# Optimization experiments

Hardware: AMD Instinct MI355X
Metric: run time of the kernel (lower is better)

The kernel has to match this reference:

```python
import jax, jax.numpy as jnp
import numpy as np

NUM_ACTIVE = 2  # num_active from init


def setup_inputs() -> dict:
    key = jax.random.key(0)
    k1, k2, k3, k4 = jax.random.split(key, 4)
    B, S, D, H, E = 2, 1024, 1024, 4096, 8
    x = jax.random.normal(k1, (B, S, D), jnp.float32)
    # router initialized to zeros in the torch module, but we use small random
    # weights so routing is non-degenerate for the correctness baseline
    router_w = jax.random.normal(k2, (D, E), jnp.float32) * 0.02
    router_b = jnp.zeros((E,), jnp.float32)
    w12 = jax.random.normal(k3, (E, D, 2 * H), jnp.float32) * (1.0 / np.sqrt(D))
    w3 = jax.random.normal(k4, (E, H, D), jnp.float32) * (1.0 / np.sqrt(H))
    return {"x": x, "router_w": router_w, "router_b": router_b, "w12": w12, "w3": w3}


def reference(x, router_w, router_b, w12, w3):
    E = router_w.shape[-1]
    # router (eval mode: no jitter noise)
    logits = x @ router_w + router_b                      # [B,S,E]
    scores = jax.nn.sigmoid(logits)
    top_s, top_i = jax.lax.top_k(scores, NUM_ACTIVE)      # [B,S,k]
    rw = top_s / (jnp.sum(top_s, axis=-1, keepdims=True) + 1e-6)
    # per-token combine weight for each expert: sum of routed slot weights
    cw = jnp.sum(jax.nn.one_hot(top_i, E, dtype=x.dtype) * rw[..., None], axis=-2)  # [B,S,E]
    # dense all-expert SwiGLU (same math as masked loop in the original)
    x12 = jnp.einsum('bsd,edh->ebsh', x, w12)             # [E,B,S,2H]
    x1, x2 = jnp.split(x12, 2, axis=-1)
    h = jax.nn.silu(x1) * x2                              # [E,B,S,H]
    out = jnp.einsum('ebsh,ehd,bse->bsd', h, w3, cw)      # [B,S,D]
    aux_loss = 0.01 * jnp.mean(logits ** 2)
    return out, aux_loss
```

## Files before the change

### kernel.cpp

```cpp
#include <hip/hip_runtime.h>
#include <hip/hip_bf16.h>

#define TOK 2048
#define DIM 1024
#define HID 4096
#define NE  8

typedef short bf16x8 __attribute__((ext_vector_type(8)));
typedef float f32x4 __attribute__((ext_vector_type(4)));
typedef unsigned short ushort_t;
typedef unsigned int uint_t;

#define SWZB(n) (((((n) >> 2) ^ ((n) >> 4)) & 3) << 4)

__device__ __forceinline__ ushort_t f2bf(float f) {
  uint_t b = __float_as_uint(f);
  uint_t r = (b + 0x7FFFu + ((b >> 16) & 1u)) >> 16;
  return (ushort_t)r;
}
__device__ __forceinline__ float bf2f(ushort_t u) {
  return __uint_as_float(((uint_t)u) << 16);
}
__device__ __forceinline__ uint_t pk2bf(float a, float b) {
  uint_t r;
  asm("v_cvt_pk_bf16_f32 %0, %1, %2" : "=v"(r) : "v"(a), "v"(b));
  return r;
}

__global__ void router_kernel(const float* __restrict__ x,
                              const float* __restrict__ rw,
                              const float* __restrict__ rb,
                              int* __restrict__ counts,
                              float* __restrict__ tok_ss,
                              int* __restrict__ top_e,
                              float* __restrict__ top_w) {
  const int t = blockIdx.x;
  const int lane = threadIdx.x;
  float acc[NE];
#pragma unroll
  for (int e = 0; e < NE; ++e) acc[e] = 0.f;
  const float* xr = x + (size_t)t * DIM;
  for (int d = lane; d < DIM; d += 64) {
    float xv = xr[d];
    const float* w = rw + (size_t)d * NE;
#pragma unroll
    for (int e = 0; e < NE; ++e) acc[e] += xv * w[e];
  }
#pragma unroll
  for (int e = 0; e < NE; ++e) {
    float v = acc[e];
#pragma unroll
    for (int off = 32; off > 0; off >>= 1) v += __shfl_down(v, off, 64);
    acc[e] = v;
  }
  if (lane == 0) {
    float sc[NE];
    float ss = 0.f;
#pragma unroll
    for (int e = 0; e < NE; ++e) {
      float lg = acc[e] + rb[e];
      ss += lg * lg;
      sc[e] = 1.f / (1.f + expf(-lg));
    }
    tok_ss[t] = ss;
    int i0 = 0;
#pragma unroll
    for (int e = 1; e < NE; ++e) if (sc[e] > sc[i0]) i0 = e;
    int i1 = (i0 == 0) ? 1 : 0;
#pragma unroll
    for (int e = 0; e < NE; ++e) if (e != i0 && sc[e] > sc[i1]) i1 = e;
    float s0 = sc[i0], s1 = sc[i1];
    float inv = 1.f / (s0 + s1 + 1e-6f);
    top_e[t * 2 + 0] = i0;
    top_e[t * 2 + 1] = i1;
    top_w[t * 2 + 0] = s0 * inv;
    top_w[t * 2 + 1] = s1 * inv;
    atomicAdd(&counts[i0], 1);
    atomicAdd(&counts[i1], 1);
  }
}

__global__ void zero_kernel(int* __restrict__ counts) {
  if (threadIdx.x < NE) counts[threadIdx.x] = 0;
}

__global__ void scan_assign_kernel(const int* __restrict__ counts,
                                   const int* __restrict__ top_e,
                                   const float* __restrict__ top_w,
                                   int* __restrict__ offsets,
                                   int* __restrict__ list_tok,
                                   float* __restrict__ list_w,
                                   int* __restrict__ pair_pos) {
  __shared__ int loff[NE + 1];
  __shared__ int lfill[NE];
  if (threadIdx.x == 0) {
    int o = 0;
    for (int e = 0; e < NE; ++e) { loff[e] = o; lfill[e] = o; o += counts[e]; }
    loff[NE] = o;
  }
  __syncthreads();
  if (threadIdx.x <= NE) offsets[threadIdx.x] = loff[threadIdx.x];
  for (int i = threadIdx.x; i < TOK * 2; i += 256) {
    int e = top_e[i];
    int idx = atomicAdd(&lfill[e], 1);
    list_tok[idx] = i >> 1;
    list_w[idx] = top_w[i];
    pair_pos[i] = idx;
  }
}

__global__ void aux_kernel(const float* __restrict__ tok_ss, float* __restrict__ out_aux) {
  __shared__ float sm[256];
  float s = 0.f;
  for (int t = threadIdx.x; t < TOK; t += 256) s += tok_ss[t];
  sm[threadIdx.x] = s;
  __syncthreads();
  for (int w = 128; w > 0; w >>= 1) {
    if (threadIdx.x < w) sm[threadIdx.x] += sm[threadIdx.x + w];
    __syncthreads();
  }
  if (threadIdx.x == 0) *out_aux = 0.01f * sm[0] / (float)(TOK * NE);
}

__global__ void convx_kernel(const float* __restrict__ x, ushort_t* __restrict__ xb) {
  int i = blockIdx.x * 256 + threadIdx.x;
  float4 v = ((const float4*)x)[i];
  uint2 u;
  u.x = pk2bf(v.x, v.y);
  u.y = pk2bf(v.z, v.w);
  ((uint2*)xb)[i] = u;
}

__global__ __launch_bounds__(256)
void gemm1_mfma(const ushort_t* __restrict__ xb,
                const float* __restrict__ w12,
                const int* __restrict__ offsets, const int* __restrict__ list_tok,
                ushort_t* __restrict__ hhi) {
  __shared__ __align__(16) ushort_t Ah[128 * 40];
  __shared__ __align__(16) ushort_t B1[64 * 40];
  __shared__ __align__(16) ushort_t B2[64 * 40];
  __shared__ int stok[128];

  const int e = blockIdx.y >> 4;
  const int rt = blockIdx.y & 15;
  const int rowstart = offsets[e] + rt * 128;
  const int rowend = offsets[e + 1];
  if (rowstart >= rowend) return;
  const int h0 = blockIdx.x * 64;
  const int tid = threadIdx.x;
  const int lane = tid & 63, wid = tid >> 6;
  const int wm = wid >> 1, wn = wid & 1;
  const int lr = lane & 15, kh = lane >> 4;

  if (tid < 128) {
    int r = rowstart + tid;
    stok[tid] = list_tok[r < rowend ? r : rowstart];
  }
  __syncthreads();

  f32x4 acc1[4][2], acc2[4][2];
#pragma unroll
  for (int mi = 0; mi < 4; ++mi)
#pragma unroll
    for (int nj = 0; nj < 2; ++nj) {
      acc1[mi][nj] = (f32x4){0.f, 0.f, 0.f, 0.f};
      acc2[mi][nj] = (f32x4){0.f, 0.f, 0.f, 0.f};
    }

  const int arow0 = tid >> 2, aseg = tid & 3;
  const int arow1 = arow0 + 64;
  const size_t asrc0 = (size_t)stok[arow0] * DIM + aseg * 8;
  const size_t asrc1 = (size_t)stok[arow1] * DIM + aseg * 8;
  const int adst0 = arow0 * 40 + aseg * 8;
  const int adst1 = arow1 * 40 + aseg * 8;

  const int p = tid >> 4, n4 = tid & 15;
  const float* w12e = w12 + (size_t)e * DIM * (2 * HID) + h0 + n4 * 4;
  char* B1c = (char*)B1;
  char* B2c = (char*)B2;

  int boff[2];
#pragma unroll
  for (int nj = 0; nj < 2; ++nj) {
    int n = wn * 32 + nj * 16 + lr;
    boff[nj] = n * 80 + ((kh * 16) ^ SWZB(n));
  }
  int bwoff[4];
#pragma unroll
  for (int c = 0; c < 4; ++c) {
    int n = n4 * 4 + c;
    bwoff[c] = n * 80 + ((4 * p) ^ SWZB(n));
  }

  uint4 ra0, ra1;
  float4 w1a, w1b, w2a, w2b;
#define G1_LOAD(K0) do { \
    ra0 = *(const uint4*)&xb[asrc0 + (K0)]; \
    ra1 = *(const uint4*)&xb[asrc1 + (K0)]; \
    const float* r0 = w12e + (size_t)((K0) + 2 * p) * (2 * HID); \
    w1a = *(const float4*)r0; \
    w1b = *(const float4*)(r0 + 2 * HID); \
    w2a = *(const float4*)(r0 + HID); \
    w2b = *(const float4*)(r0 + HID + 2 * HID); \
  } while (0)

  G1_LOAD(0);
#pragma unroll 1
  for (int k0 = 0; k0 < DIM; k0 += 32) {
    *(uint4*)&Ah[adst0] = ra0;
    *(uint4*)&Ah[adst1] = ra1;
    {
      const float* p1a = (const float*)&w1a;
      const float* p1b = (const float*)&w1b;
      const float* p2a = (const float*)&w2a;
      const float* p2b = (const float*)&w2b;
#pragma unroll
      for (int c = 0; c < 4; ++c) {
        *(uint_t*)(B1c + bwoff[c]) = pk2bf(p1a[c], p1b[c]);
        *(uint_t*)(B2c + bwoff[c]) = pk2bf(p2a[c], p2b[c]);
      }
    }
    __syncthreads();
    if (k0 + 32 < DIM) G1_LOAD(k0 + 32);

    bf16x8 af[4], b1f[2], b2f[2];
#pragma unroll
    for (int mi = 0; mi < 4; ++mi)
      af[mi] = *(bf16x8*)&Ah[(wm * 64 + mi * 16 + lr) * 40 + kh * 8];
#pragma unroll
    for (int nj = 0; nj < 2; ++nj) {
      b1f[nj] = *(bf16x8*)(B1c + boff[nj]);
      b2f[nj] = *(bf16x8*)(B2c + boff[nj]);
    }
#pragma unroll
    for (int mi = 0; mi < 4; ++mi)
#pragma unroll
      for (int nj = 0; nj < 2; ++nj) {
        acc1[mi][nj] = __builtin_amdgcn_mfma_f32_16x16x32_bf16(af[mi], b1f[nj], acc1[mi][nj], 0, 0, 0);
        acc2[mi][nj] = __builtin_amdgcn_mfma_f32_16x16x32_bf16(af[mi], b2f[nj], acc2[mi][nj], 0, 0, 0);
      }
    __syncthreads();
  }
#undef G1_LOAD

#pragma unroll
  for (int mi = 0; mi < 4; ++mi)
#pragma unroll
    for (int nj = 0; nj < 2; ++nj)
#pragma unroll
      for (int r = 0; r < 4; ++r) {
        int row_t = wm * 64 + mi * 16 + kh * 4 + r;
        int gr = rowstart + row_t;
        if (gr < rowend) {
          int col = h0 + wn * 32 + nj * 16 + lr;
          float v1 = acc1[mi][nj][r], v2 = acc2[mi][nj][r];
          float hv = (v1 / (1.f + expf(-v1))) * v2;
          hhi[(size_t)gr * HID + col] = f2bf(hv);
        }
      }
}

__global__ __launch_bounds__(256)
void gemm2_mfma(const ushort_t* __restrict__ hhi,
                const float* __restrict__ w3,
                const int* __restrict__ offsets, const float* __restrict__ list_w,
                ushort_t* __restrict__ pairout) {
  __shared__ __align__(16) ushort_t As0[64 * 40];
  __shared__ __align__(16) ushort_t As1[64 * 40];
  __shared__ __align__(16) ushort_t Bs0[64 * 40];
  __shared__ __align__(16) ushort_t Bs1[64 * 40];

  const int e = blockIdx.y >> 4;
  const int rt = blockIdx.y & 15;
  const int rowstart = offsets[e] + rt * 64;
  const int rowend = offsets[e + 1];
  if (rowstart >= rowend) return;
  const int d0 = blockIdx.x * 64;
  const int tid = threadIdx.x;
  const int lane = tid & 63, wid = tid >> 6;
  const int wm = wid >> 1, wn = wid & 1;
  const int lr = lane & 15, kh = lane >> 4;

  f32x4 acc[2][2];
#pragma unroll
  for (int mi = 0; mi < 2; ++mi)
#pragma unroll
    for (int nj = 0; nj < 2; ++nj) acc[mi][nj] = (f32x4){0.f, 0.f, 0.f, 0.f};

  const int arow = tid >> 2, aseg = tid & 3;
  int gr = rowstart + arow; if (gr >= rowend) gr = rowstart;
  const size_t asrc = (size_t)gr * HID + aseg * 8;
  const int adst = arow * 40 + aseg * 8;

  const int p = tid >> 4, n4 = tid & 15;
  const float* w3e = w3 + (size_t)e * HID * DIM + d0 + n4 * 4;
  char* Bs0c = (char*)Bs0;
  char* Bs1c = (char*)Bs1;

  int boff[2];
#pragma unroll
  for (int nj = 0; nj < 2; ++nj) {
    int n = wn * 32 + nj * 16 + lr;
    boff[nj] = n * 80 + ((kh * 16) ^ SWZB(n));
  }
  int bwoff[4];
#pragma unroll
  for (int c = 0; c < 4; ++c) {
    int n = n4 * 4 + c;
    bwoff[c] = n * 80 + ((4 * p) ^ SWZB(n));
  }

  uint4 ra0, ra1;
  float4 rb00, rb01, rb10, rb11;
#define G2_LOAD(K0) do { \
    ra0 = *(const uint4*)&hhi[asrc + (K0)]; \
    ra1 = *(const uint4*)&hhi[asrc + (K0) + 32]; \
    const float* r0 = w3e + (size_t)((K0) + 2 * p) * DIM; \
    rb00 = *(const float4*)r0; \
    rb01 = *(const float4*)(r0 + DIM); \
    const float* r1 = w3e + (size_t)((K0) + 32 + 2 * p) * DIM; \
    rb10 = *(const float4*)r1; \
    rb11 = *(const float4*)(r1 + DIM); \
  } while (0)

  G2_LOAD(0);
#pragma unroll 1
  for (int k0 = 0; k0 < HID; k0 += 64) {
    *(uint4*)&As0[adst] = ra0;
    *(uint4*)&As1[adst] = ra1;
    {
      const float* pv0 = (const float*)&rb00;
      const float* pv1 = (const float*)&rb01;
      const float* pw0 = (const float*)&rb10;
      const float* pw1 = (const float*)&rb11;
#pragma unroll
      for (int c = 0; c < 4; ++c) {
        *(uint_t*)(Bs0c + bwoff[c]) = pk2bf(pv0[c], pv1[c]);
        *(uint_t*)(Bs1c + bwoff[c]) = pk2bf(pw0[c], pw1[c]);
      }
    }
    __syncthreads();
    if (k0 + 64 < HID) G2_LOAD(k0 + 64);

    {
      bf16x8 af[2], bf[2];
#pragma unroll
      for (int mi = 0; mi < 2; ++mi)
        af[mi] = *(bf16x8*)&As0[(wm * 32 + mi * 16 + lr) * 40 + kh * 8];
#pragma unroll
      for (int nj = 0; nj < 2; ++nj)
        bf[nj] = *(bf16x8*)(Bs0c + boff[nj]);
#pragma unroll
      for (int mi = 0; mi < 2; ++mi)
#pragma unroll
        for (int nj = 0; nj < 2; ++nj)
          acc[mi][nj] = __builtin_amdgcn_mfma_f32_16x16x32_bf16(af[mi], bf[nj], acc[mi][nj], 0, 0, 0);
    }
    {
      bf16x8 af[2], bf[2];
#pragma unroll
      for (int mi = 0; mi < 2; ++mi)
        af[mi] = *(bf16x8*)&As1[(wm * 32 + mi * 16 + lr) * 40 + kh * 8];
#pragma unroll
      for (int nj = 0; nj < 2; ++nj)
        bf[nj] = *(bf16x8*)(Bs1c + boff[nj]);
#pragma unroll
      for (int mi = 0; mi < 2; ++mi)
#pragma unroll
        for (int nj = 0; nj < 2; ++nj)
          acc[mi][nj] = __builtin_amdgcn_mfma_f32_16x16x32_bf16(af[mi], bf[nj], acc[mi][nj], 0, 0, 0);
    }
    __syncthreads();
  }
#undef G2_LOAD

#pragma unroll
  for (int mi = 0; mi < 2; ++mi)
#pragma unroll
    for (int nj = 0; nj < 2; ++nj)
#pragma unroll
      for (int r = 0; r < 4; ++r) {
        int grr = rowstart + wm * 32 + mi * 16 + kh * 4 + r;
        if (grr < rowend) {
          int col = d0 + wn * 32 + nj * 16 + lr;
          pairout[(size_t)grr * DIM + col] = f2bf(acc[mi][nj][r] * list_w[grr]);
        }
      }
}

__global__ void combine_bf(const ushort_t* __restrict__ pairout,
                           const int* __restrict__ pair_pos,
                           float* __restrict__ out) {
  int i = blockIdx.x * 256 + threadIdx.x;
  int t = i >> 8;
  int dv = i & 255;
  int p0 = pair_pos[2 * t], p1 = pair_pos[2 * t + 1];
  ushort4 a = *(const ushort4*)&pairout[(size_t)p0 * DIM + dv * 4];
  ushort4 b = *(const ushort4*)&pairout[(size_t)p1 * DIM + dv * 4];
  float4 o;
  o.x = bf2f(a.x) + bf2f(b.x);
  o.y = bf2f(a.y) + bf2f(b.y);
  o.z = bf2f(a.z) + bf2f(b.z);
  o.w = bf2f(a.w) + bf2f(b.w);
  ((float4*)out)[i] = o;
}

extern "C" void kernel_launch(void* const* d_in, const int* in_sizes, int n_in,
                              void* d_out, int out_size, void* d_ws, size_t ws_size,
                              hipStream_t stream) {
  const float* x   = (const float*)d_in[0];
  const float* rw  = (const float*)d_in[1];
  const float* rb  = (const float*)d_in[2];
  const float* w12 = (const float*)d_in[3];
  const float* w3  = (const float*)d_in[4];
  float* out = (float*)d_out;

  char* ws = (char*)d_ws;
  size_t off = 0;
  auto alloc = [&](size_t bytes) {
    void* p = ws + off;
    off = (off + bytes + 255) & ~255ULL;
    return p;
  };
  int*   counts   = (int*)alloc(NE * 4);
  int*   offsets  = (int*)alloc((NE + 1) * 4);
  float* tok_ss   = (float*)alloc(TOK * 4);
  int*   top_e    = (int*)alloc(TOK * 2 * 4);
  float* top_w    = (float*)alloc(TOK * 2 * 4);
  int*   list_tok = (int*)alloc(TOK * 2 * 4);
  float* list_w   = (float*)alloc(TOK * 2 * 4);
  int*   pair_pos = (int*)alloc(TOK * 2 * 4);

  ushort_t* xb      = (ushort_t*)alloc((size_t)TOK * DIM * 2);
  ushort_t* hhi     = (ushort_t*)alloc((size_t)TOK * 2 * HID * 2);
  ushort_t* pairoutb= (ushort_t*)alloc((size_t)TOK * 2 * DIM * 2);

  hipLaunchKernelGGL(zero_kernel, dim3(1), dim3(64), 0, stream, counts);
  hipLaunchKernelGGL(router_kernel, dim3(TOK), dim3(64), 0, stream,
                     x, rw, rb, counts, tok_ss, top_e, top_w);
  hipLaunchKernelGGL(scan_assign_kernel, dim3(1), dim3(256), 0, stream,
                     counts, top_e, top_w, offsets, list_tok, list_w, pair_pos);
  hipLaunchKernelGGL(aux_kernel, dim3(1), dim3(256), 0, stream,
                     tok_ss, out + (size_t)TOK * DIM);

  hipLaunchKernelGGL(convx_kernel, dim3(TOK * DIM / 4 / 256), dim3(256), 0, stream,
                     x, xb);
  hipLaunchKernelGGL(gemm1_mfma, dim3(HID / 64, NE * 16), dim3(256), 0, stream,
                     xb, w12, offsets, list_tok, hhi);
  hipLaunchKernelGGL(gemm2_mfma, dim3(DIM / 64, NE * 16), dim3(256), 0, stream,
                     hhi, w3, offsets, list_w, pairoutb);
  hipLaunchKernelGGL(combine_bf, dim3(TOK * DIM / 4 / 256), dim3(256), 0, stream,
                     pairoutb, pair_pos, out);
}
```

Before: 341.0 us.

## Double-buffer LDS tiles in both expert GEMM kernels

Both grouped GEMM kernels now keep two LDS buffers for the A and B tiles. Each step computes from the current buffer, then stores the already-prefetched registers into the other buffer and issues the next global load. The goal is to separate LDS writes from MFMA reads and keep loads in flight over more of the loop. The loop still has two barriers per iteration, and the doubled LDS footprint may reduce how many blocks fit on a CU.

```diff
diff --git a/kernel.cpp b/kernel.cpp
--- a/kernel.cpp
+++ b/kernel.cpp
@@ -136,9 +136,9 @@
                 const float* __restrict__ w12,
                 const int* __restrict__ offsets, const int* __restrict__ list_tok,
                 ushort_t* __restrict__ hhi) {
-  __shared__ __align__(16) ushort_t Ah[128 * 40];
-  __shared__ __align__(16) ushort_t B1[64 * 40];
-  __shared__ __align__(16) ushort_t B2[64 * 40];
+  __shared__ __align__(16) ushort_t Ah[2][128 * 40];
+  __shared__ __align__(16) ushort_t B1[2][64 * 40];
+  __shared__ __align__(16) ushort_t B2[2][64 * 40];
   __shared__ int stok[128];
 
   const int e = blockIdx.y >> 4;
@@ -176,8 +176,6 @@
 
   const int p = tid >> 4, n4 = tid & 15;
   const float* w12e = w12 + (size_t)e * DIM * (2 * HID) + h0 + n4 * 4;
-  char* B1c = (char*)B1;
-  char* B2c = (char*)B2;
 
   int boff[2];
 #pragma unroll
@@ -203,34 +201,41 @@
     w2a = *(const float4*)(r0 + HID); \
     w2b = *(const float4*)(r0 + HID + 2 * HID); \
   } while (0)
-
+#define G1_STORE(BUF) do { \
+    *(uint4*)&Ah[BUF][adst0] = ra0; \
+    *(uint4*)&Ah[BUF][adst1] = ra1; \
+    char* b1c = (char*)B1[BUF]; \
+    char* b2c = (char*)B2[BUF]; \
+    const float* p1a = (const float*)&w1a; \
+    const float* p1b = (const float*)&w1b; \
+    const float* p2a = (const float*)&w2a; \
+    const float* p2b = (const float*)&w2b; \
+    _Pragma("unroll") \
+    for (int c = 0; c < 4; ++c) { \
+      *(uint_t*)(b1c + bwoff[c]) = pk2bf(p1a[c], p1b[c]); \
+      *(uint_t*)(b2c + bwoff[c]) = pk2bf(p2a[c], p2b[c]); \
+    } } while (0)
+
+  const int NK = DIM / 32;
   G1_LOAD(0);
+  G1_STORE(0);
+  G1_LOAD(32);
+  __syncthreads();
+  int cur = 0;
+
 #pragma unroll 1
-  for (int k0 = 0; k0 < DIM; k0 += 32) {
-    *(uint4*)&Ah[adst0] = ra0;
-    *(uint4*)&Ah[adst1] = ra1;
-    {
-      const float* p1a = (const float*)&w1a;
-      const float* p1b = (const float*)&w1b;
-      const float* p2a = (const float*)&w2a;
-      const float* p2b = (const float*)&w2b;
-#pragma unroll
-      for (int c = 0; c < 4; ++c) {
-        *(uint_t*)(B1c + bwoff[c]) = pk2bf(p1a[c], p1b[c]);
-        *(uint_t*)(B2c + bwoff[c]) = pk2bf(p2a[c], p2b[c]);
-      }
-    }
-    __syncthreads();
-    if (k0 + 32 < DIM) G1_LOAD(k0 + 32);
-
+  for (int step = 0; step < NK; ++step) {
+    const char* b1r = (const char*)B1[cur];
+    const char* b2r = (const char*)B2[cur];
+    const ushort_t* ahr = Ah[cur];
     bf16x8 af[4], b1f[2], b2f[2];
 #pragma unroll
     for (int mi = 0; mi < 4; ++mi)
-      af[mi] = *(bf16x8*)&Ah[(wm * 64 + mi * 16 + lr) * 40 + kh * 8];
+      af[mi] = *(const bf16x8*)&ahr[(wm * 64 + mi * 16 + lr) * 40 + kh * 8];
 #pragma unroll
     for (int nj = 0; nj < 2; ++nj) {
-      b1f[nj] = *(bf16x8*)(B1c + boff[nj]);
-      b2f[nj] = *(bf16x8*)(B2c + boff[nj]);
+      b1f[nj] = *(const bf16x8*)(b1r + boff[nj]);
+      b2f[nj] = *(const bf16x8*)(b2r + boff[nj]);
     }
 #pragma unroll
     for (int mi = 0; mi < 4; ++mi)
@@ -239,9 +244,16 @@
         acc1[mi][nj] = __builtin_amdgcn_mfma_f32_16x16x32_bf16(af[mi], b1f[nj], acc1[mi][nj], 0, 0, 0);
         acc2[mi][nj] = __builtin_amdgcn_mfma_f32_16x16x32_bf16(af[mi], b2f[nj], acc2[mi][nj], 0, 0, 0);
       }
-    __syncthreads();
+    if (step + 1 < NK) {
+      __syncthreads();
+      G1_STORE(cur ^ 1);
+      if (step + 2 < NK) G1_LOAD((step + 2) * 32);
+      __syncthreads();
+      cur ^= 1;
+    }
   }
 #undef G1_LOAD
+#undef G1_STORE
 
 #pragma unroll
   for (int mi = 0; mi < 4; ++mi)
@@ -265,10 +277,10 @@
                 const float* __restrict__ w3,
                 const int* __restrict__ offsets, const float* __restrict__ list_w,
                 ushort_t* __restrict__ pairout) {
-  __shared__ __align__(16) ushort_t As0[64 * 40];
-  __shared__ __align__(16) ushort_t As1[64 * 40];
-  __shared__ __align__(16) ushort_t Bs0[64 * 40];
-  __shared__ __align__(16) ushort_t Bs1[64 * 40];
+  __shared__ __align__(16) ushort_t As0[2][64 * 40];
+  __shared__ __align__(16) ushort_t As1[2][64 * 40];
+  __shared__ __align__(16) ushort_t Bs0[2][64 * 40];
+  __shared__ __align__(16) ushort_t Bs1[2][64 * 40];
 
   const int e = blockIdx.y >> 4;
   const int rt = blockIdx.y & 15;
@@ -294,8 +306,6 @@
 
   const int p = tid >> 4, n4 = tid & 15;
   const float* w3e = w3 + (size_t)e * HID * DIM + d0 + n4 * 4;
-  char* Bs0c = (char*)Bs0;
-  char* Bs1c = (char*)Bs1;
 
   int boff[2];
 #pragma unroll
@@ -322,34 +332,40 @@
     rb10 = *(const float4*)r1; \
     rb11 = *(const float4*)(r1 + DIM); \
   } while (0)
-
+#define G2_STORE(BUF) do { \
+    *(uint4*)&As0[BUF][adst] = ra0; \
+    *(uint4*)&As1[BUF][adst] = ra1; \
+    char* bs0c = (char*)Bs0[BUF]; \
+    char* bs1c = (char*)Bs1[BUF]; \
+    const float* pv0 = (const float*)&rb00; \
+    const float* pv1 = (const float*)&rb01; \
+    const float* pw0 = (const float*)&rb10; \
+    const float* pw1 = (const float*)&rb11; \
+    _Pragma("unroll") \
+    for (int c = 0; c < 4; ++c) { \
+      *(uint_t*)(bs0c + bwoff[c]) = pk2bf(pv0[c], pv1[c]); \
+      *(uint_t*)(bs1c + bwoff[c]) = pk2bf(pw0[c], pw1[c]); \
+    } } while (0)
+
+  const int NT = HID / 64;
   G2_LOAD(0);
+  G2_STORE(0);
+  G2_LOAD(64);
+  __syncthreads();
+  int cur = 0;
+
 #pragma unroll 1
-  for (int k0 = 0; k0 < HID; k0 += 64) {
-    *(uint4*)&As0[adst] = ra0;
-    *(uint4*)&As1[adst] = ra1;
+  for (int step = 0; step < NT; ++step) {
     {
-      const float* pv0 = (const float*)&rb00;
-      const float* pv1 = (const float*)&rb01;
-      const float* pw0 = (const float*)&rb10;
-      const float* pw1 = (const float*)&rb11;
-#pragma unroll
-      for (int c = 0; c < 4; ++c) {
-        *(uint_t*)(Bs0c + bwoff[c]) = pk2bf(pv0[c], pv1[c]);
-        *(uint_t*)(Bs1c + bwoff[c]) = pk2bf(pw0[c], pw1[c]);
-      }
-    }
-    __syncthreads();
-    if (k0 + 64 < HID) G2_LOAD(k0 + 64);
-
-    {
+      const ushort_t* asr = As0[cur];
+      const char* bsr = (const char*)Bs0[cur];
       bf16x8 af[2], bf[2];
 #pragma unroll
       for (int mi = 0; mi < 2; ++mi)
-        af[mi] = *(bf16x8*)&As0[(wm * 32 + mi * 16 + lr) * 40 + kh * 8];
+        af[mi] = *(const bf16x8*)&asr[(wm * 32 + mi * 16 + lr) * 40 + kh * 8];
 #pragma unroll
       for (int nj = 0; nj < 2; ++nj)
-        bf[nj] = *(bf16x8*)(Bs0c + boff[nj]);
+        bf[nj] = *(const bf16x8*)(bsr + boff[nj]);
 #pragma unroll
       for (int mi = 0; mi < 2; ++mi)
 #pragma unroll
@@ -357,22 +373,31 @@
           acc[mi][nj] = __builtin_amdgcn_mfma_f32_16x16x32_bf16(af[mi], bf[nj], acc[mi][nj], 0, 0, 0);
     }
     {
+      const ushort_t* asr = As1[cur];
+      const char* bsr = (const char*)Bs1[cur];
       bf16x8 af[2], bf[2];
 #pragma unroll
       for (int mi = 0; mi < 2; ++mi)
-        af[mi] = *(bf16x8*)&As1[(wm * 32 + mi * 16 + lr) * 40 + kh * 8];
+        af[mi] = *(const bf16x8*)&asr[(wm * 32 + mi * 16 + lr) * 40 + kh * 8];
 #pragma unroll
       for (int nj = 0; nj < 2; ++nj)
-        bf[nj] = *(bf16x8*)(Bs1c + boff[nj]);
+        bf[nj] = *(const bf16x8*)(bsr + boff[nj]);
 #pragma unroll
       for (int mi = 0; mi < 2; ++mi)
 #pragma unroll
         for (int nj = 0; nj < 2; ++nj)
           acc[mi][nj] = __builtin_amdgcn_mfma_f32_16x16x32_bf16(af[mi], bf[nj], acc[mi][nj], 0, 0, 0);
     }
-    __syncthreads();
+    if (step + 1 < NT) {
+      __syncthreads();
+      G2_STORE(cur ^ 1);
+      if (step + 2 < NT) G2_LOAD((step + 2) * 64);
+      __syncthreads();
+      cur ^= 1;
+    }
   }
 #undef G2_LOAD
+#undef G2_STORE
 
 #pragma unroll
   for (int mi = 0; mi < 2; ++mi)
```

New measurement: 342.0 us. About the same (+0.3%).

## Widen gemm1 N-tile to 128, fuse bf16 conversion into router, drop count kernels

Applied to the files above, without the earlier changes.

gemm1 now computes a 128-wide hidden tile per block instead of 64, doubling the per-block accumulators and B staging in shared memory. Each gathered x tile is reused across twice as many columns, which halves the redundant A reads but raises register pressure. The router kernel now also writes the bf16 copy of x, removing the separate convx launch. Per-expert counts are now computed in shared memory inside scan_assign, removing zero_kernel and the global atomics.

```diff
diff --git a/kernel.cpp b/kernel.cpp
--- a/kernel.cpp
+++ b/kernel.cpp
@@ -30,21 +30,31 @@
 __global__ void router_kernel(const float* __restrict__ x,
                               const float* __restrict__ rw,
                               const float* __restrict__ rb,
-                              int* __restrict__ counts,
                               float* __restrict__ tok_ss,
                               int* __restrict__ top_e,
-                              float* __restrict__ top_w) {
+                              float* __restrict__ top_w,
+                              ushort_t* __restrict__ xb) {
   const int t = blockIdx.x;
   const int lane = threadIdx.x;
   float acc[NE];
 #pragma unroll
   for (int e = 0; e < NE; ++e) acc[e] = 0.f;
-  const float* xr = x + (size_t)t * DIM;
-  for (int d = lane; d < DIM; d += 64) {
-    float xv = xr[d];
-    const float* w = rw + (size_t)d * NE;
-#pragma unroll
-    for (int e = 0; e < NE; ++e) acc[e] += xv * w[e];
+  const float4* x4 = (const float4*)(x + (size_t)t * DIM);
+  uint2* xb2 = (uint2*)(xb + (size_t)t * DIM);
+#pragma unroll
+  for (int j = 0; j < 4; ++j) {
+    int i = j * 64 + lane;
+    float4 v = x4[i];
+    uint2 u;
+    u.x = pk2bf(v.x, v.y);
+    u.y = pk2bf(v.z, v.w);
+    xb2[i] = u;
+    const float* w = rw + (size_t)i * 4 * NE;
+    const float* vp = (const float*)&v;
+#pragma unroll
+    for (int c = 0; c < 4; ++c)
+#pragma unroll
+      for (int e = 0; e < NE; ++e) acc[e] += vp[c] * w[c * NE + e];
   }
 #pragma unroll
   for (int e = 0; e < NE; ++e) {
@@ -75,27 +85,26 @@
     top_e[t * 2 + 1] = i1;
     top_w[t * 2 + 0] = s0 * inv;
     top_w[t * 2 + 1] = s1 * inv;
-    atomicAdd(&counts[i0], 1);
-    atomicAdd(&counts[i1], 1);
-  }
-}
-
-__global__ void zero_kernel(int* __restrict__ counts) {
-  if (threadIdx.x < NE) counts[threadIdx.x] = 0;
-}
-
-__global__ void scan_assign_kernel(const int* __restrict__ counts,
-                                   const int* __restrict__ top_e,
+  }
+}
+
+__global__ void scan_assign_kernel(const int* __restrict__ top_e,
                                    const float* __restrict__ top_w,
                                    int* __restrict__ offsets,
                                    int* __restrict__ list_tok,
                                    float* __restrict__ list_w,
                                    int* __restrict__ pair_pos) {
+  __shared__ int lcount[NE];
   __shared__ int loff[NE + 1];
   __shared__ int lfill[NE];
+  if (threadIdx.x < NE) lcount[threadIdx.x] = 0;
+  __syncthreads();
+  for (int i = threadIdx.x; i < TOK * 2; i += 256)
+    atomicAdd(&lcount[top_e[i]], 1);
+  __syncthreads();
   if (threadIdx.x == 0) {
     int o = 0;
-    for (int e = 0; e < NE; ++e) { loff[e] = o; lfill[e] = o; o += counts[e]; }
+    for (int e = 0; e < NE; ++e) { loff[e] = o; lfill[e] = o; o += lcount[e]; }
     loff[NE] = o;
   }
   __syncthreads();
@@ -122,23 +131,14 @@
   if (threadIdx.x == 0) *out_aux = 0.01f * sm[0] / (float)(TOK * NE);
 }
 
-__global__ void convx_kernel(const float* __restrict__ x, ushort_t* __restrict__ xb) {
-  int i = blockIdx.x * 256 + threadIdx.x;
-  float4 v = ((const float4*)x)[i];
-  uint2 u;
-  u.x = pk2bf(v.x, v.y);
-  u.y = pk2bf(v.z, v.w);
-  ((uint2*)xb)[i] = u;
-}
-
 __global__ __launch_bounds__(256)
 void gemm1_mfma(const ushort_t* __restrict__ xb,
                 const float* __restrict__ w12,
                 const int* __restrict__ offsets, const int* __restrict__ list_tok,
                 ushort_t* __restrict__ hhi) {
   __shared__ __align__(16) ushort_t Ah[128 * 40];
-  __shared__ __align__(16) ushort_t B1[64 * 40];
-  __shared__ __align__(16) ushort_t B2[64 * 40];
+  __shared__ __align__(16) ushort_t B1[128 * 40];
+  __shared__ __align__(16) ushort_t B2[128 * 40];
   __shared__ int stok[128];
 
   const int e = blockIdx.y >> 4;
@@ -146,7 +146,7 @@
   const int rowstart = offsets[e] + rt * 128;
   const int rowend = offsets[e + 1];
   if (rowstart >= rowend) return;
-  const int h0 = blockIdx.x * 64;
+  const int h0 = blockIdx.x * 128;
   const int tid = threadIdx.x;
   const int lane = tid & 63, wid = tid >> 6;
   const int wm = wid >> 1, wn = wid & 1;
@@ -158,11 +158,11 @@
   }
   __syncthreads();
 
-  f32x4 acc1[4][2], acc2[4][2];
+  f32x4 acc1[4][4], acc2[4][4];
 #pragma unroll
   for (int mi = 0; mi < 4; ++mi)
 #pragma unroll
-    for (int nj = 0; nj < 2; ++nj) {
+    for (int nj = 0; nj < 4; ++nj) {
       acc1[mi][nj] = (f32x4){0.f, 0.f, 0.f, 0.f};
       acc2[mi][nj] = (f32x4){0.f, 0.f, 0.f, 0.f};
     }
@@ -179,29 +179,35 @@
   char* B1c = (char*)B1;
   char* B2c = (char*)B2;
 
-  int boff[2];
-#pragma unroll
-  for (int nj = 0; nj < 2; ++nj) {
-    int n = wn * 32 + nj * 16 + lr;
+  int boff[4];
+#pragma unroll
+  for (int nj = 0; nj < 4; ++nj) {
+    int n = wn * 64 + nj * 16 + lr;
     boff[nj] = n * 80 + ((kh * 16) ^ SWZB(n));
   }
-  int bwoff[4];
+  int bwoff[4], bwoff2[4];
 #pragma unroll
   for (int c = 0; c < 4; ++c) {
     int n = n4 * 4 + c;
     bwoff[c] = n * 80 + ((4 * p) ^ SWZB(n));
+    int n2 = 64 + n;
+    bwoff2[c] = n2 * 80 + ((4 * p) ^ SWZB(n2));
   }
 
   uint4 ra0, ra1;
-  float4 w1a, w1b, w2a, w2b;
+  float4 w1a, w1b, w1c, w1d, w2a, w2b, w2c, w2d;
 #define G1_LOAD(K0) do { \
     ra0 = *(const uint4*)&xb[asrc0 + (K0)]; \
     ra1 = *(const uint4*)&xb[asrc1 + (K0)]; \
     const float* r0 = w12e + (size_t)((K0) + 2 * p) * (2 * HID); \
     w1a = *(const float4*)r0; \
     w1b = *(const float4*)(r0 + 2 * HID); \
+    w1c = *(const float4*)(r0 + 64); \
+    w1d = *(const float4*)(r0 + 2 * HID + 64); \
     w2a = *(const float4*)(r0 + HID); \
     w2b = *(const float4*)(r0 + HID + 2 * HID); \
+    w2c = *(const float4*)(r0 + HID + 64); \
+    w2d = *(const float4*)(r0 + HID + 2 * HID + 64); \
   } while (0)
 
   G1_LOAD(0);
@@ -212,30 +218,36 @@
     {
       const float* p1a = (const float*)&w1a;
       const float* p1b = (const float*)&w1b;
+      const float* p1c = (const float*)&w1c;
+      const float* p1d = (const float*)&w1d;
       const float* p2a = (const float*)&w2a;
       const float* p2b = (const float*)&w2b;
+      const float* p2c = (const float*)&w2c;
+      const float* p2d = (const float*)&w2d;
 #pragma unroll
       for (int c = 0; c < 4; ++c) {
-        *(uint_t*)(B1c + bwoff[c]) = pk2bf(p1a[c], p1b[c]);
-        *(uint_t*)(B2c + bwoff[c]) = pk2bf(p2a[c], p2b[c]);
+        *(uint_t*)(B1c + bwoff[c])  = pk2bf(p1a[c], p1b[c]);
+        *(uint_t*)(B2c + bwoff[c])  = pk2bf(p2a[c], p2b[c]);
+        *(uint_t*)(B1c + bwoff2[c]) = pk2bf(p1c[c], p1d[c]);
+        *(uint_t*)(B2c + bwoff2[c]) = pk2bf(p2c[c], p2d[c]);
       }
     }
     __syncthreads();
     if (k0 + 32 < DIM) G1_LOAD(k0 + 32);
 
-    bf16x8 af[4], b1f[2], b2f[2];
+    bf16x8 af[4], b1f[4], b2f[4];
 #pragma unroll
     for (int mi = 0; mi < 4; ++mi)
       af[mi] = *(bf16x8*)&Ah[(wm * 64 + mi * 16 + lr) * 40 + kh * 8];
 #pragma unroll
-    for (int nj = 0; nj < 2; ++nj) {
+    for (int nj = 0; nj < 4; ++nj) {
       b1f[nj] = *(bf16x8*)(B1c + boff[nj]);
       b2f[nj] = *(bf16x8*)(B2c + boff[nj]);
     }
 #pragma unroll
     for (int mi = 0; mi < 4; ++mi)
 #pragma unroll
-      for (int nj = 0; nj < 2; ++nj) {
+      for (int nj = 0; nj < 4; ++nj) {
         acc1[mi][nj] = __builtin_amdgcn_mfma_f32_16x16x32_bf16(af[mi], b1f[nj], acc1[mi][nj], 0, 0, 0);
         acc2[mi][nj] = __builtin_amdgcn_mfma_f32_16x16x32_bf16(af[mi], b2f[nj], acc2[mi][nj], 0, 0, 0);
       }
@@ -246,13 +258,13 @@
 #pragma unroll
   for (int mi = 0; mi < 4; ++mi)
 #pragma unroll
-    for (int nj = 0; nj < 2; ++nj)
+    for (int nj = 0; nj < 4; ++nj)
 #pragma unroll
       for (int r = 0; r < 4; ++r) {
         int row_t = wm * 64 + mi * 16 + kh * 4 + r;
         int gr = rowstart + row_t;
         if (gr < rowend) {
-          int col = h0 + wn * 32 + nj * 16 + lr;
+          int col = h0 + wn * 64 + nj * 16 + lr;
           float v1 = acc1[mi][nj][r], v2 = acc2[mi][nj][r];
           float hv = (v1 / (1.f + expf(-v1))) * v2;
           hhi[(size_t)gr * HID + col] = f2bf(hv);
@@ -323,6 +335,7 @@
     rb11 = *(const float4*)(r1 + DIM); \
   } while (0)
 
+  const int NT = HID / 64;
   G2_LOAD(0);
 #pragma unroll 1
   for (int k0 = 0; k0 < HID; k0 += 64) {
@@ -422,7 +435,6 @@
     off = (off + bytes + 255) & ~255ULL;
     return p;
   };
-  int*   counts   = (int*)alloc(NE * 4);
   int*   offsets  = (int*)alloc((NE + 1) * 4);
   float* tok_ss   = (float*)alloc(TOK * 4);
   int*   top_e    = (int*)alloc(TOK * 2 * 4);
@@ -435,17 +447,14 @@
   ushort_t* hhi     = (ushort_t*)alloc((size_t)TOK * 2 * HID * 2);
   ushort_t* pairoutb= (ushort_t*)alloc((size_t)TOK * 2 * DIM * 2);
 
-  hipLaunchKernelGGL(zero_kernel, dim3(1), dim3(64), 0, stream, counts);
   hipLaunchKernelGGL(router_kernel, dim3(TOK), dim3(64), 0, stream,
-                     x, rw, rb, counts, tok_ss, top_e, top_w);
+                     x, rw, rb, tok_ss, top_e, top_w, xb);
   hipLaunchKernelGGL(scan_assign_kernel, dim3(1), dim3(256), 0, stream,
-                     counts, top_e, top_w, offsets, list_tok, list_w, pair_pos);
+                     top_e, top_w, offsets, list_tok, list_w, pair_pos);
   hipLaunchKernelGGL(aux_kernel, dim3(1), dim3(256), 0, stream,
                      tok_ss, out + (size_t)TOK * DIM);
 
-  hipLaunchKernelGGL(convx_kernel, dim3(TOK * DIM / 4 / 256), dim3(256), 0, stream,
-                     x, xb);
-  hipLaunchKernelGGL(gemm1_mfma, dim3(HID / 64, NE * 16), dim3(256), 0, stream,
+  hipLaunchKernelGGL(gemm1_mfma, dim3(HID / 128, NE * 16), dim3(256), 0, stream,
                      xb, w12, offsets, list_tok, hhi);
   hipLaunchKernelGGL(gemm2_mfma, dim3(DIM / 64, NE * 16), dim3(256), 0, stream,
                      hhi, w3, offsets, list_w, pairoutb);
```

New measurement: 356.4 us. +4.5%, slower.

## Fuse x conversion into router, count in scan, scatter-add gemm2 output

Applied to the files above, without the earlier changes.

Folds the fp32-to-bf16 conversion of x into the router kernel, so each token row is read once. Expert counting moves into the scan kernel's shared memory, which removes the zero kernel and the global atomics. gemm2 now atomically adds weighted results straight into the fp32 output, so the pairout buffer and combine kernel go away; the output is cleared with a memset, and the gemm2 grid is doubled in row tiles so heavily loaded experts are fully covered. In exchange it adds float atomics on the output, which make the summation order nondeterministic, and extra blocks that exit early.

```diff
diff --git a/kernel.cpp b/kernel.cpp
--- a/kernel.cpp
+++ b/kernel.cpp
@@ -30,21 +30,31 @@
 __global__ void router_kernel(const float* __restrict__ x,
                               const float* __restrict__ rw,
                               const float* __restrict__ rb,
-                              int* __restrict__ counts,
                               float* __restrict__ tok_ss,
                               int* __restrict__ top_e,
-                              float* __restrict__ top_w) {
+                              float* __restrict__ top_w,
+                              ushort_t* __restrict__ xb) {
   const int t = blockIdx.x;
   const int lane = threadIdx.x;
   float acc[NE];
 #pragma unroll
   for (int e = 0; e < NE; ++e) acc[e] = 0.f;
-  const float* xr = x + (size_t)t * DIM;
-  for (int d = lane; d < DIM; d += 64) {
-    float xv = xr[d];
-    const float* w = rw + (size_t)d * NE;
-#pragma unroll
-    for (int e = 0; e < NE; ++e) acc[e] += xv * w[e];
+  const float4* x4 = (const float4*)(x + (size_t)t * DIM);
+  uint2* xb2 = (uint2*)(xb + (size_t)t * DIM);
+#pragma unroll
+  for (int j = 0; j < 4; ++j) {
+    int i = j * 64 + lane;
+    float4 v = x4[i];
+    uint2 u;
+    u.x = pk2bf(v.x, v.y);
+    u.y = pk2bf(v.z, v.w);
+    xb2[i] = u;
+    const float* w = rw + (size_t)i * 4 * NE;
+    const float* vp = (const float*)&v;
+#pragma unroll
+    for (int c = 0; c < 4; ++c)
+#pragma unroll
+      for (int e = 0; e < NE; ++e) acc[e] += vp[c] * w[c * NE + e];
   }
 #pragma unroll
   for (int e = 0; e < NE; ++e) {
@@ -75,27 +85,25 @@
     top_e[t * 2 + 1] = i1;
     top_w[t * 2 + 0] = s0 * inv;
     top_w[t * 2 + 1] = s1 * inv;
-    atomicAdd(&counts[i0], 1);
-    atomicAdd(&counts[i1], 1);
-  }
-}
-
-__global__ void zero_kernel(int* __restrict__ counts) {
-  if (threadIdx.x < NE) counts[threadIdx.x] = 0;
-}
-
-__global__ void scan_assign_kernel(const int* __restrict__ counts,
-                                   const int* __restrict__ top_e,
+  }
+}
+
+__global__ void scan_assign_kernel(const int* __restrict__ top_e,
                                    const float* __restrict__ top_w,
                                    int* __restrict__ offsets,
                                    int* __restrict__ list_tok,
-                                   float* __restrict__ list_w,
-                                   int* __restrict__ pair_pos) {
+                                   float* __restrict__ list_w) {
+  __shared__ int lcount[NE];
   __shared__ int loff[NE + 1];
   __shared__ int lfill[NE];
+  if (threadIdx.x < NE) lcount[threadIdx.x] = 0;
+  __syncthreads();
+  for (int i = threadIdx.x; i < TOK * 2; i += 256)
+    atomicAdd(&lcount[top_e[i]], 1);
+  __syncthreads();
   if (threadIdx.x == 0) {
     int o = 0;
-    for (int e = 0; e < NE; ++e) { loff[e] = o; lfill[e] = o; o += counts[e]; }
+    for (int e = 0; e < NE; ++e) { loff[e] = o; lfill[e] = o; o += lcount[e]; }
     loff[NE] = o;
   }
   __syncthreads();
@@ -105,7 +113,6 @@
     int idx = atomicAdd(&lfill[e], 1);
     list_tok[idx] = i >> 1;
     list_w[idx] = top_w[i];
-    pair_pos[i] = idx;
   }
 }
 
@@ -120,15 +127,6 @@
     __syncthreads();
   }
   if (threadIdx.x == 0) *out_aux = 0.01f * sm[0] / (float)(TOK * NE);
-}
-
-__global__ void convx_kernel(const float* __restrict__ x, ushort_t* __restrict__ xb) {
-  int i = blockIdx.x * 256 + threadIdx.x;
-  float4 v = ((const float4*)x)[i];
-  uint2 u;
-  u.x = pk2bf(v.x, v.y);
-  u.y = pk2bf(v.z, v.w);
-  ((uint2*)xb)[i] = u;
 }
 
 __global__ __launch_bounds__(256)
@@ -264,14 +262,15 @@
 void gemm2_mfma(const ushort_t* __restrict__ hhi,
                 const float* __restrict__ w3,
                 const int* __restrict__ offsets, const float* __restrict__ list_w,
-                ushort_t* __restrict__ pairout) {
+                const int* __restrict__ list_tok,
+                float* __restrict__ out) {
   __shared__ __align__(16) ushort_t As0[64 * 40];
   __shared__ __align__(16) ushort_t As1[64 * 40];
   __shared__ __align__(16) ushort_t Bs0[64 * 40];
   __shared__ __align__(16) ushort_t Bs1[64 * 40];
 
-  const int e = blockIdx.y >> 4;
-  const int rt = blockIdx.y & 15;
+  const int e = blockIdx.y >> 5;
+  const int rt = blockIdx.y & 31;
   const int rowstart = offsets[e] + rt * 64;
   const int rowend = offsets[e + 1];
   if (rowstart >= rowend) return;
@@ -383,26 +382,10 @@
         int grr = rowstart + wm * 32 + mi * 16 + kh * 4 + r;
         if (grr < rowend) {
           int col = d0 + wn * 32 + nj * 16 + lr;
-          pairout[(size_t)grr * DIM + col] = f2bf(acc[mi][nj][r] * list_w[grr]);
+          int tok = list_tok[grr];
+          atomicAdd(&out[(size_t)tok * DIM + col], acc[mi][nj][r] * list_w[grr]);
         }
       }
-}
-
-__global__ void combine_bf(const ushort_t* __restrict__ pairout,
-                           const int* __restrict__ pair_pos,
-                           float* __restrict__ out) {
-  int i = blockIdx.x * 256 + threadIdx.x;
-  int t = i >> 8;
-  int dv = i & 255;
-  int p0 = pair_pos[2 * t], p1 = pair_pos[2 * t + 1];
-  ushort4 a = *(const ushort4*)&pairout[(size_t)p0 * DIM + dv * 4];
-  ushort4 b = *(const ushort4*)&pairout[(size_t)p1 * DIM + dv * 4];
-  float4 o;
-  o.x = bf2f(a.x) + bf2f(b.x);
-  o.y = bf2f(a.y) + bf2f(b.y);
-  o.z = bf2f(a.z) + bf2f(b.z);
-  o.w = bf2f(a.w) + bf2f(b.w);
-  ((float4*)out)[i] = o;
 }
 
 extern "C" void kernel_launch(void* const* d_in, const int* in_sizes, int n_in,
@@ -422,33 +405,27 @@
     off = (off + bytes + 255) & ~255ULL;
     return p;
   };
-  int*   counts   = (int*)alloc(NE * 4);
   int*   offsets  = (int*)alloc((NE + 1) * 4);
   float* tok_ss   = (float*)alloc(TOK * 4);
   int*   top_e    = (int*)alloc(TOK * 2 * 4);
   float* top_w    = (float*)alloc(TOK * 2 * 4);
   int*   list_tok = (int*)alloc(TOK * 2 * 4);
   float* list_w   = (float*)alloc(TOK * 2 * 4);
-  int*   pair_pos = (int*)alloc(TOK * 2 * 4);
-
-  ushort_t* xb      = (ushort_t*)alloc((size_t)TOK * DIM * 2);
-  ushort_t* hhi     = (ushort_t*)alloc((size_t)TOK * 2 * HID * 2);
-  ushort_t* pairoutb= (ushort_t*)alloc((size_t)TOK * 2 * DIM * 2);
-
-  hipLaunchKernelGGL(zero_kernel, dim3(1), dim3(64), 0, stream, counts);
+
+  ushort_t* xb  = (ushort_t*)alloc((size_t)TOK * DIM * 2);
+  ushort_t* hhi = (ushort_t*)alloc((size_t)TOK * 2 * HID * 2);
+
+  hipMemsetAsync(out, 0, (size_t)TOK * DIM * 4, stream);
+
   hipLaunchKernelGGL(router_kernel, dim3(TOK), dim3(64), 0, stream,
-                     x, rw, rb, counts, tok_ss, top_e, top_w);
+                     x, rw, rb, tok_ss, top_e, top_w, xb);
   hipLaunchKernelGGL(scan_assign_kernel, dim3(1), dim3(256), 0, stream,
-                     counts, top_e, top_w, offsets, list_tok, list_w, pair_pos);
+                     top_e, top_w, offsets, list_tok, list_w);
   hipLaunchKernelGGL(aux_kernel, dim3(1), dim3(256), 0, stream,
                      tok_ss, out + (size_t)TOK * DIM);
 
-  hipLaunchKernelGGL(convx_kernel, dim3(TOK * DIM / 4 / 256), dim3(256), 0, stream,
-                     x, xb);
   hipLaunchKernelGGL(gemm1_mfma, dim3(HID / 64, NE * 16), dim3(256), 0, stream,
                      xb, w12, offsets, list_tok, hhi);
-  hipLaunchKernelGGL(gemm2_mfma, dim3(DIM / 64, NE * 16), dim3(256), 0, stream,
-                     hhi, w3, offsets, list_w, pairoutb);
-  hipLaunchKernelGGL(combine_bf, dim3(TOK * DIM / 4 / 256), dim3(256), 0, stream,
-                     pairoutb, pair_pos, out);
-}
+  hipLaunchKernelGGL(gemm2_mfma, dim3(DIM / 64, NE * 32), dim3(256), 0, stream,
+                     hhi, w3, offsets, list_w, list_tok, out);
+}
```

Result: faster. 303.1 us (-11.1%).
